# Kernel tuning notes

Hardware: AMD Instinct MI355X
Metric: run time of the kernel (lower is better)

## Reference

```python
import jax, jax.numpy as jnp
import numpy as np
from jax.scipy.linalg import solve_triangular

REG = 1e-6  # reg_covar added to covariance diagonal
LOG2PI = float(np.log(2.0 * np.pi))
RESP_EPS = 10.0 * float(np.finfo(np.float32).eps)


def _log_gauss(X, means, covs):
    # X: [N,D], means: [K,D], covs: [K,D,D] -> per-sample per-component log N(x|mu_k, Sigma_k): [N,K]
    K, D = means.shape
    eye = jnp.eye(D, dtype=X.dtype)
    chol = jnp.linalg.cholesky(covs + REG * eye)                      # [K,D,D]
    diff = X[None, :, :] - means[:, None, :]                          # [K,N,D]
    sol = jax.vmap(lambda L, d: solve_triangular(L, d.T, lower=True))(chol, diff)  # [K,D,N]
    maha = jnp.sum(sol * sol, axis=1)                                 # [K,N]
    logdet = jnp.sum(jnp.log(jnp.diagonal(chol, axis1=1, axis2=2)), axis=1)  # [K] = 0.5*log|Sigma|
    return (-0.5 * (D * LOG2PI + maha) - logdet[:, None]).T           # [N,K]


def _em_step(X, weights, means, covs):
    N, D = X.shape
    # E-step: responsibilities via stable logsumexp
    lp = _log_gauss(X, means, covs) + jnp.log(weights)[None, :]       # [N,K]
    log_norm = jax.scipy.special.logsumexp(lp, axis=1)                # [N]
    resp = jnp.exp(lp - log_norm[:, None])                            # [N,K]
    # M-step (MLE)
    nk = resp.sum(axis=0) + RESP_EPS                                  # [K]
    new_w = nk / N
    new_means = (resp.T @ X) / nk[:, None]                            # [K,D]
    diff = X[None, :, :] - new_means[:, None, :]                      # [K,N,D]
    new_covs = jnp.einsum('kn,knd,kne->kde', resp.T, diff, diff) / nk[:, None, None]
    new_covs = new_covs + REG * jnp.eye(D, dtype=X.dtype)
    return new_w, new_means, new_covs


def reference(X, weights, means, covariances, n_iter):
    # Normalize provided weights (uniform init in the torch module)
    w0 = weights / jnp.sum(weights)

    def step(carry, _):
        w, m, c = carry
        return _em_step(X, w, m, c), None

    (w, m, c), _ = jax.lax.scan(step, (w0, means, covariances), xs=None, length=n_iter)
    # Final per-sample log-likelihood under the fitted mixture (lower bound)
    lp = _log_gauss(X, m, c) + jnp.log(w)[None, :]
    return jax.scipy.special.logsumexp(lp, axis=1)                    # [N]


def setup_inputs() -> dict:
    key = jax.random.key(0)
    kx, km = jax.random.split(key)
    N, D, K = 100000, 32, 16
    X = jax.random.normal(kx, (N, D), dtype=jnp.float32)
    weights = jnp.ones((K,), dtype=jnp.float32) / K
    means = jax.random.normal(km, (K, D), dtype=jnp.float32)
    covariances = jnp.tile(jnp.eye(D, dtype=jnp.float32)[None], (K, 1, 1))
    return {"X": X, "weights": weights, "means": means, "covariances": covariances, "n_iter": 5}
```

## Files before the change

### kernel.cpp

```cpp
#include <hip/hip_runtime.h>
#include <math.h>

#define REGC 1e-6f
#define LOG2PI 1.83787706640934534f
#define RESP_EPS 1.1920929e-6f

#define PART_K 1156
#define RS 16

typedef __attribute__((ext_vector_type(8))) short short8;
typedef __attribute__((ext_vector_type(4))) float f32x4;
typedef unsigned short ushort_t;
typedef unsigned int uint_t;

__device__ __forceinline__ ushort_t f2bf(float x) {
    uint_t u = __float_as_uint(x);
    uint_t r = (u + 0x7fffu + ((u >> 16) & 1u)) >> 16;
    return (ushort_t)r;
}
__device__ __forceinline__ float bf2f(ushort_t h) {
    return __uint_as_float(((uint_t)h) << 16);
}
__device__ __forceinline__ f32x4 shx4(f32x4 v, int m) {
    f32x4 r;
#pragma unroll
    for (int i = 0; i < 4; ++i) r[i] = __shfl_xor(v[i], m);
    return r;
}
__device__ __forceinline__ f32x4 sel4(bool s, f32x4 b, f32x4 a) {
    f32x4 r;
#pragma unroll
    for (int i = 0; i < 4; ++i) r[i] = s ? b[i] : a[i];
    return r;
}
__device__ __forceinline__ short8 pack_rx(const float* r8, const short8 bh, float& row) {
    uint_t u[8];
#pragma unroll
    for (int jj = 0; jj < 8; ++jj) {
        float av = r8[jj] * bf2f((ushort_t)bh[jj]);
        row += av;
        u[jj] = __float_as_uint(av) + 0x8000u;
    }
    short8 out;
    uint_t* o = (uint_t*)&out;
    o[0] = __builtin_amdgcn_perm(u[1], u[0], 0x07060302);
    o[1] = __builtin_amdgcn_perm(u[3], u[2], 0x07060302);
    o[2] = __builtin_amdgcn_perm(u[5], u[4], 0x07060302);
    o[3] = __builtin_amdgcn_perm(u[7], u[6], 0x07060302);
    return out;
}

__global__ __launch_bounds__(256) void gmm_xsplit(const float* __restrict__ X,
                                                  ushort_t* __restrict__ Xh,
                                                  ushort_t* __restrict__ Xl,
                                                  ushort_t* __restrict__ XTH,
                                                  int N) {
    int chunk = blockIdx.x;
    int t = threadIdx.x;
    __shared__ float xsh[32][33];
    int s = t >> 3, q = t & 7;
    int n = chunk * 32 + s;
    float4 v = make_float4(0.f, 0.f, 0.f, 0.f);
    if (n < N) v = ((const float4*)(X + (size_t)n * 32))[q];
    float vv[4] = { v.x, v.y, v.z, v.w };
    xsh[s][q * 4 + 0] = v.x; xsh[s][q * 4 + 1] = v.y;
    xsh[s][q * 4 + 2] = v.z; xsh[s][q * 4 + 3] = v.w;
    if (n < N) {
        ushort_t h[4], l[4];
#pragma unroll
        for (int i = 0; i < 4; ++i) {
            h[i] = f2bf(vv[i]);
            l[i] = f2bf(vv[i] - bf2f(h[i]));
        }
        size_t o = (size_t)n * 32 + q * 4;
        *(uint2*)(Xh + o) = make_uint2((uint_t)h[0] | ((uint_t)h[1] << 16),
                                       (uint_t)h[2] | ((uint_t)h[3] << 16));
        *(uint2*)(Xl + o) = make_uint2((uint_t)l[0] | ((uint_t)l[1] << 16),
                                       (uint_t)l[2] | ((uint_t)l[3] << 16));
    }
    __syncthreads();
    int di = t >> 7;
    int lane = (t >> 1) & 63;
    int jj0 = (t & 1) * 4;
    int c = lane & 15, quad = lane >> 4;
    int d = di * 16 + c;
    ushort_t fh[4];
#pragma unroll
    for (int i = 0; i < 4; ++i) fh[i] = f2bf(xsh[quad * 8 + jj0 + i][d]);
    size_t fo = ((size_t)(chunk * 2 + di) * 64 + lane) * 8 + jj0;
    *(uint2*)(XTH + fo) = make_uint2((uint_t)fh[0] | ((uint_t)fh[1] << 16),
                                     (uint_t)fh[2] | ((uint_t)fh[3] << 16));
}

__global__ __launch_bounds__(64) void gmm_prep0(const float* __restrict__ w,
                                                const float* __restrict__ mu,
                                                const float* __restrict__ cov,
                                                ushort_t* __restrict__ Wh,
                                                ushort_t* __restrict__ Wl,
                                                float* __restrict__ Bv,
                                                float* __restrict__ Cc) {
    int k = blockIdx.x;
    int t = threadIdx.x;
    __shared__ float L[32][33];
    __shared__ float Ai[32][33];
    const float* cv = cov + (size_t)k * 1024;
    const float* muk = mu + (size_t)k * 32;
#pragma unroll
    for (int rep = 0; rep < 16; ++rep) {
        int idx = rep * 64 + t;
        int i = idx >> 5, j = idx & 31;
        L[i][j] = cv[idx] + (i == j ? REGC : 0.f);
    }
    __syncthreads();
#pragma unroll
    for (int j = 0; j < 32; ++j) {
        float s = L[j][j];
#pragma unroll
        for (int p = 0; p < j; ++p) { float v = L[j][p]; s -= v * v; }
        float dj = sqrtf(s);
        if (t > j && t < 32) {
            float s2 = L[t][j];
#pragma unroll
            for (int p = 0; p < j; ++p) s2 -= L[t][p] * L[j][p];
            L[t][j] = s2 / dj;
        }
        if (t == j) L[j][j] = dj;
        __syncthreads();
    }
    if (t < 32) {
        float ai[32];
#pragma unroll
        for (int r = 0; r < 32; ++r) {
            float s = (r == t) ? 1.f : 0.f;
#pragma unroll
            for (int p = 0; p < r; ++p) s -= L[r][p] * ai[p];
            ai[r] = s / L[r][r];
        }
#pragma unroll
        for (int r = 0; r < 32; ++r) Ai[r][t] = ai[r];
    }
    __syncthreads();
#pragma unroll
    for (int rep = 0; rep < 16; ++rep) {
        int idx = rep * 64 + t;
        int i = idx >> 5, j = idx & 31;
        float v = Ai[i][j];
        ushort_t h = f2bf(v);
        Wh[(size_t)(k * 32 + i) * 32 + j] = h;
        Wl[(size_t)(k * 32 + i) * 32 + j] = f2bf(v - bf2f(h));
    }
    if (t < 32) {
        float s = 0.f;
#pragma unroll
        for (int j = 0; j < 32; ++j) s += Ai[t][j] * muk[j];
        Bv[k * 32 + t] = s;
    }
    float wsum = 0.f;
#pragma unroll
    for (int i = 0; i < 16; ++i) wsum += w[i];
    float lv = (t < 32) ? logf(L[t & 31][t & 31]) : 0.f;
#pragma unroll
    for (int off = 1; off < 32; off <<= 1) lv += __shfl_xor(lv, off);
    if (t == 0) Cc[k] = logf(w[k] / wsum) - 0.5f * 32.0f * LOG2PI - lv;
}

__global__ __launch_bounds__(1024) __attribute__((amdgpu_waves_per_eu(4, 4)))
void gmm_emstep(const ushort_t* __restrict__ Xh, const ushort_t* __restrict__ Xl,
                const ushort_t* __restrict__ XTH,
                const ushort_t* __restrict__ Wh, const ushort_t* __restrict__ Wl,
                const float* __restrict__ Bv, const float* __restrict__ Cc,
                float* __restrict__ part, int N) {
    __shared__ float rsh[16][516];
    int t = threadIdx.x;
    int wave = t >> 6, lane = t & 63;
    int quad = lane >> 4, c = lane & 15;

    int wstart0 = (int)blockIdx.x * 512 + wave * 32;
    bool dup = (wstart0 + 32 > N);
    int wst = dup ? ((N >= 32) ? N - 32 : 0) : wstart0;

    size_t xo0 = (size_t)(wst + c) * 32 + quad * 8;
    size_t xo1 = (size_t)(wst + 16 + c) * 32 + quad * 8;
    short8 ah0 = *(const short8*)(Xh + xo0);
    short8 al0 = *(const short8*)(Xl + xo0);
    short8 ah1 = *(const short8*)(Xh + xo1);
    short8 al1 = *(const short8*)(Xl + xo1);

    {
        f32x4 p0[2], p1[2], p2[2], p3[2], fin[2];
#pragma unroll
        for (int k = 0; k < 16; ++k) {
            size_t w0 = (size_t)(k * 32 + c) * 32 + quad * 8;
            size_t w1 = w0 + 512;
            short8 bh0 = *(const short8*)(Wh + w0);
            short8 bl0 = *(const short8*)(Wl + w0);
            short8 bh1 = *(const short8*)(Wh + w1);
            short8 bl1 = *(const short8*)(Wl + w1);
            float bv0 = Bv[k * 32 + c];
            float bv1 = Bv[k * 32 + 16 + c];
#pragma unroll
            for (int tt = 0; tt < 2; ++tt) {
                short8 ah = tt ? ah1 : ah0;
                short8 al = tt ? al1 : al0;
                f32x4 a0 = {0.f, 0.f, 0.f, 0.f};
                f32x4 a1 = {0.f, 0.f, 0.f, 0.f};
                a0 = __builtin_amdgcn_mfma_f32_16x16x32_bf16(ah, bh0, a0, 0, 0, 0);
                a0 = __builtin_amdgcn_mfma_f32_16x16x32_bf16(ah, bl0, a0, 0, 0, 0);
                a0 = __builtin_amdgcn_mfma_f32_16x16x32_bf16(al, bh0, a0, 0, 0, 0);
                a1 = __builtin_amdgcn_mfma_f32_16x16x32_bf16(ah, bh1, a1, 0, 0, 0);
                a1 = __builtin_amdgcn_mfma_f32_16x16x32_bf16(ah, bl1, a1, 0, 0, 0);
                a1 = __builtin_amdgcn_mfma_f32_16x16x32_bf16(al, bh1, a1, 0, 0, 0);
                f32x4 ms;
#pragma unroll
                for (int r = 0; r < 4; ++r) {
                    float d0 = a0[r] - bv0;
                    float d1 = a1[r] - bv1;
                    ms[r] = fmaf(d0, d0, d1 * d1);
                }
                if ((k & 1) == 0) { p0[tt] = ms; }
                else {
                    f32x4 a = p0[tt] + shx4(p0[tt], 1);
                    f32x4 b = ms + shx4(ms, 1);
                    f32x4 v = sel4((c & 1) != 0, b, a);
                    if ((k & 2) == 0) { p1[tt] = v; }
                    else {
                        a = p1[tt] + shx4(p1[tt], 2); b = v + shx4(v, 2); v = sel4((c & 2) != 0, b, a);
                        if ((k & 4) == 0) { p2[tt] = v; }
                        else {
                            a = p2[tt] + shx4(p2[tt], 4); b = v + shx4(v, 4); v = sel4((c & 4) != 0, b, a);
                            if ((k & 8) == 0) { p3[tt] = v; }
                            else {
                                a = p3[tt] + shx4(p3[tt], 8); b = v + shx4(v, 8);
                                fin[tt] = sel4((c & 8) != 0, b, a);
                            }
                        }
                    }
                }
            }
        }
        float ccv = Cc[c];
#pragma unroll
        for (int tt = 0; tt < 2; ++tt) {
            f32x4 lp;
#pragma unroll
            for (int r = 0; r < 4; ++r) lp[r] = ccv - 0.5f * fin[tt][r];
            f32x4 mx = lp;
#pragma unroll
            for (int off = 1; off < 16; off <<= 1) {
                f32x4 s = shx4(mx, off);
#pragma unroll
                for (int r = 0; r < 4; ++r) mx[r] = fmaxf(mx[r], s[r]);
            }
            f32x4 e;
#pragma unroll
            for (int r = 0; r < 4; ++r) e[r] = __expf(lp[r] - mx[r]);
            f32x4 sm = e;
#pragma unroll
            for (int off = 1; off < 16; off <<= 1) sm = sm + shx4(sm, off);
            f32x4 sv;
#pragma unroll
            for (int r = 0; r < 4; ++r) sv[r] = dup ? 0.f : e[r] / sm[r];
            *(f32x4*)&rsh[c][wave * 32 + tt * 16 + quad * 4] = sv;
        }
    }
    __syncthreads();

    {
        int k = wave;
        f32x4 m00 = {0.f,0.f,0.f,0.f}, m01 = {0.f,0.f,0.f,0.f};
        f32x4 m10 = {0.f,0.f,0.f,0.f}, m11 = {0.f,0.f,0.f,0.f};
        float row0 = 0.f, row1 = 0.f, corner = 0.f;
#pragma unroll 4
        for (int ch = 0; ch < 16; ++ch) {
            size_t fb = (((size_t)((int)blockIdx.x * 16 + ch)) * 128 + lane) * 8;
            short8 bh0 = *(const short8*)(XTH + fb);
            short8 bh1 = *(const short8*)(XTH + fb + 512);
            float r8[8];
#pragma unroll
            for (int jj = 0; jj < 8; ++jj) r8[jj] = rsh[k][ch * 32 + quad * 8 + jj];
            corner += ((r8[0]+r8[1])+(r8[2]+r8[3])) + ((r8[4]+r8[5])+(r8[6]+r8[7]));
            short8 a0 = pack_rx(r8, bh0, row0);
            short8 a1 = pack_rx(r8, bh1, row1);
            m00 = __builtin_amdgcn_mfma_f32_16x16x32_bf16(a0, bh0, m00, 0, 0, 0);
            m01 = __builtin_amdgcn_mfma_f32_16x16x32_bf16(a0, bh1, m01, 0, 0, 0);
            m10 = __builtin_amdgcn_mfma_f32_16x16x32_bf16(a1, bh0, m10, 0, 0, 0);
            m11 = __builtin_amdgcn_mfma_f32_16x16x32_bf16(a1, bh1, m11, 0, 0, 0);
        }
        row0 += __shfl_xor(row0, 16);  row0 += __shfl_xor(row0, 32);
        row1 += __shfl_xor(row1, 16);  row1 += __shfl_xor(row1, 32);
        corner += __shfl_xor(corner, 16);  corner += __shfl_xor(corner, 32);

        float* pb = part + ((size_t)blockIdx.x * 16 + k) * PART_K;
#pragma unroll
        for (int r = 0; r < 4; ++r) {
            pb[(quad * 4 + r) * 34 + c]           = m00[r];
            pb[(quad * 4 + r) * 34 + 16 + c]      = m01[r];
            pb[(16 + quad * 4 + r) * 34 + c]      = m10[r];
            pb[(16 + quad * 4 + r) * 34 + 16 + c] = m11[r];
        }
        if (quad == 0) {
            pb[32 * 34 + c]      = row0;
            pb[32 * 34 + 16 + c] = row1;
        }
        if (lane == 0) pb[32 * 34 + 32] = corner;
    }
}

__global__ __launch_bounds__(256) void gmm_reduce1(const float* __restrict__ part,
                                                   float* __restrict__ part2,
                                                   int npart) {
    int k = blockIdx.x, g = blockIdx.y;
    int nb = (npart + RS - 1) / RS;
    int b0 = g * nb;
    int b1 = b0 + nb; if (b1 > npart) b1 = npart;
    for (int idx = threadIdx.x; idx < PART_K; idx += 256) {
        float s = 0.f;
#pragma unroll 4
        for (int b = b0; b < b1; ++b)
            s += part[((size_t)b * 16 + k) * PART_K + idx];
        part2[((size_t)g * 16 + k) * PART_K + idx] = s;
    }
}

__global__ __launch_bounds__(1024) void gmm_redfin_prep(const float* __restrict__ part2,
                                                        ushort_t* __restrict__ Wh,
                                                        ushort_t* __restrict__ Wl,
                                                        float* __restrict__ Bv,
                                                        float* __restrict__ Cc,
                                                        int N) {
    int k = blockIdx.x;
    int t = threadIdx.x;
    __shared__ float S[1156];
    __shared__ float L[1056];
    __shared__ float Ai[1056];
    __shared__ float mean[32];

    for (int idx = t; idx < 1121; idx += 1024) {
        float s = 0.f;
#pragma unroll
        for (int b = 0; b < RS; ++b)
            s += part2[((size_t)b * 16 + k) * PART_K + idx];
        S[idx] = s;
    }
    __syncthreads();
    float nk = S[32 * 34 + 32] + RESP_EPS;
    float inv = 1.f / nk;
    {
        int i = t >> 5, j = t & 31;
        float mi = S[32 * 34 + i] * inv;
        float mj = S[32 * 34 + j] * inv;
        L[i * 33 + j] = S[i * 34 + j] * inv - mi * mj + ((i == j) ? 2.f * REGC : 0.f);
    }
    if (t < 32) mean[t] = S[32 * 34 + t] * inv;
    __syncthreads();

#pragma unroll
    for (int j = 0; j < 32; ++j) {
        if (t < 32) {
            float s = L[j * 33 + j];
#pragma unroll
            for (int p = 0; p < j; ++p) { float v = L[j * 33 + p]; s -= v * v; }
            float dj = sqrtf(s);
            if (t > j) {
                float s2 = L[t * 33 + j];
#pragma unroll
                for (int p = 0; p < j; ++p) s2 -= L[t * 33 + p] * L[j * 33 + p];
                L[t * 33 + j] = s2 / dj;
            }
            if (t == j) L[j * 33 + j] = dj;
        }
        __syncthreads();
    }
    if (t < 32) {
        float ai[32];
#pragma unroll
        for (int r = 0; r < 32; ++r) {
            float s = (r == t) ? 1.f : 0.f;
#pragma unroll
            for (int p = 0; p < r; ++p) s -= L[r * 33 + p] * ai[p];
            ai[r] = s / L[r * 33 + r];
        }
#pragma unroll
        for (int r = 0; r < 32; ++r) Ai[r * 33 + t] = ai[r];
    }
    __syncthreads();
    {
        int i = t >> 5, j = t & 31;
        float v = Ai[i * 33 + j];
        ushort_t h = f2bf(v);
        Wh[(size_t)(k * 32 + i) * 32 + j] = h;
        Wl[(size_t)(k * 32 + i) * 32 + j] = f2bf(v - bf2f(h));
    }
    if (t < 32) {
        float s = 0.f;
#pragma unroll
        for (int j = 0; j < 32; ++j) s += Ai[t * 33 + j] * mean[j];
        Bv[k * 32 + t] = s;
    }
    float lv = (t < 32) ? logf(L[(t & 31) * 33 + (t & 31)]) : 0.f;
#pragma unroll
    for (int off = 1; off < 32; off <<= 1) lv += __shfl_xor(lv, off);
    if (t == 0) Cc[k] = logf(nk / (float)N) - 0.5f * 32.0f * LOG2PI - lv;
}

__global__ __launch_bounds__(256, 2) void gmm_estep_fin(const ushort_t* __restrict__ Xh,
                                                        const ushort_t* __restrict__ Xl,
                                                        const ushort_t* __restrict__ Wh,
                                                        const ushort_t* __restrict__ Wl,
                                                        const float* __restrict__ Bv,
                                                        const float* __restrict__ Cc,
                                                        float* __restrict__ out,
                                                        int N) {
    int t = threadIdx.x;
    int wave = t >> 6, lane = t & 63;
    int quad = lane >> 4, c = lane & 15;
    int wstart = (blockIdx.x * 4 + wave) * 32;
    if (wstart + 32 > N) wstart = (N >= 32) ? (N - 32) : 0;
    bool al4 = ((N & 3) == 0);

    size_t xo0 = (size_t)(wstart + c) * 32 + quad * 8;
    size_t xo1 = (size_t)(wstart + 16 + c) * 32 + quad * 8;
    short8 ah0 = *(const short8*)(Xh + xo0);
    short8 al0 = *(const short8*)(Xl + xo0);
    short8 ah1 = *(const short8*)(Xh + xo1);
    short8 al1 = *(const short8*)(Xl + xo1);

    f32x4 p0[2], p1[2], p2[2], p3[2], fin[2];
#pragma unroll
    for (int k = 0; k < 16; ++k) {
        size_t w0 = (size_t)(k * 32 + c) * 32 + quad * 8;
        size_t w1 = w0 + 512;
        short8 bh0 = *(const short8*)(Wh + w0);
        short8 bl0 = *(const short8*)(Wl + w0);
        short8 bh1 = *(const short8*)(Wh + w1);
        short8 bl1 = *(const short8*)(Wl + w1);
        float bv0 = Bv[k * 32 + c];
        float bv1 = Bv[k * 32 + 16 + c];
#pragma unroll
        for (int tt = 0; tt < 2; ++tt) {
            short8 ah = tt ? ah1 : ah0;
            short8 al = tt ? al1 : al0;
            f32x4 a0 = {0.f, 0.f, 0.f, 0.f};
            f32x4 a1 = {0.f, 0.f, 0.f, 0.f};
            a0 = __builtin_amdgcn_mfma_f32_16x16x32_bf16(ah, bh0, a0, 0, 0, 0);
            a0 = __builtin_amdgcn_mfma_f32_16x16x32_bf16(ah, bl0, a0, 0, 0, 0);
            a0 = __builtin_amdgcn_mfma_f32_16x16x32_bf16(al, bh0, a0, 0, 0, 0);
            a1 = __builtin_amdgcn_mfma_f32_16x16x32_bf16(ah, bh1, a1, 0, 0, 0);
            a1 = __builtin_amdgcn_mfma_f32_16x16x32_bf16(ah, bl1, a1, 0, 0, 0);
            a1 = __builtin_amdgcn_mfma_f32_16x16x32_bf16(al, bh1, a1, 0, 0, 0);
            f32x4 ms;
#pragma unroll
            for (int r = 0; r < 4; ++r) {
                float d0 = a0[r] - bv0;
                float d1 = a1[r] - bv1;
                ms[r] = fmaf(d0, d0, d1 * d1);
            }
            if ((k & 1) == 0) { p0[tt] = ms; }
            else {
                f32x4 a = p0[tt] + shx4(p0[tt], 1);
                f32x4 b = ms + shx4(ms, 1);
                f32x4 v = sel4((c & 1) != 0, b, a);
                if ((k & 2) == 0) { p1[tt] = v; }
                else {
                    a = p1[tt] + shx4(p1[tt], 2); b = v + shx4(v, 2); v = sel4((c & 2) != 0, b, a);
                    if ((k & 4) == 0) { p2[tt] = v; }
                    else {
                        a = p2[tt] + shx4(p2[tt], 4); b = v + shx4(v, 4); v = sel4((c & 4) != 0, b, a);
                        if ((k & 8) == 0) { p3[tt] = v; }
                        else {
                            a = p3[tt] + shx4(p3[tt], 8); b = v + shx4(v, 8);
                            fin[tt] = sel4((c & 8) != 0, b, a);
                        }
                    }
                }
            }
        }
    }
    float ccv = Cc[c];
#pragma unroll
    for (int tt = 0; tt < 2; ++tt) {
        f32x4 lp;
#pragma unroll
        for (int r = 0; r < 4; ++r) lp[r] = ccv - 0.5f * fin[tt][r];
        f32x4 mx = lp;
#pragma unroll
        for (int off = 1; off < 16; off <<= 1) {
            f32x4 s = shx4(mx, off);
#pragma unroll
            for (int r = 0; r < 4; ++r) mx[r] = fmaxf(mx[r], s[r]);
        }
        f32x4 e;
#pragma unroll
        for (int r = 0; r < 4; ++r) e[r] = __expf(lp[r] - mx[r]);
        f32x4 sm = e;
#pragma unroll
        for (int off = 1; off < 16; off <<= 1) sm = sm + shx4(sm, off);
        if (c == 0) {
            int nb = wstart + tt * 16 + quad * 4;
            f32x4 o;
#pragma unroll
            for (int r = 0; r < 4; ++r) o[r] = mx[r] + __logf(sm[r]);
            if (al4) *(f32x4*)(out + nb) = o;
            else { for (int r = 0; r < 4; ++r) out[nb + r] = o[r]; }
        }
    }
}

extern "C" void kernel_launch(void* const* d_in, const int* in_sizes, int n_in,
                              void* d_out, int out_size, void* d_ws, size_t ws_size,
                              hipStream_t stream) {
    const float* X   = (const float*)d_in[0];
    const float* w   = (const float*)d_in[1];
    const float* mu  = (const float*)d_in[2];
    const float* cov = (const float*)d_in[3];
    const int NITER = 5;
    int N = in_sizes[0] / 32;
    int NB = (N + 511) / 512;
    int NCB = NB * 16;

    float* ws = (float*)d_ws;
    float*    Bv = ws;
    float*    Cc = ws + 512;
    ushort_t* Wh = (ushort_t*)(ws + 528);
    ushort_t* Wl = (ushort_t*)(ws + 8720);
    ushort_t* Xh = (ushort_t*)(ws + 16912);
    ushort_t* Xl = (ushort_t*)(ws + 16912 + (size_t)16 * N);
    size_t xt0 = 16912 + (size_t)32 * N;
    size_t SZ  = (size_t)NCB * 512;
    ushort_t* XTH = (ushort_t*)(ws + xt0);
    float*  part2 = ws + xt0 + SZ;
    float*  part  = part2 + (size_t)RS * 16 * PART_K;

    float* out = (float*)d_out;

    int eblocks = ((N + 31) / 32 + 3) / 4;

    gmm_xsplit<<<NCB, 256, 0, stream>>>(X, Xh, Xl, XTH, N);
    gmm_prep0<<<16, 64, 0, stream>>>(w, mu, cov, Wh, Wl, Bv, Cc);

    for (int it = 0; it < NITER; ++it) {
        gmm_emstep<<<NB, 1024, 0, stream>>>(Xh, Xl, XTH, Wh, Wl, Bv, Cc, part, N);
        dim3 r1(16, RS);
        gmm_reduce1<<<r1, 256, 0, stream>>>(part, part2, NB);
        gmm_redfin_prep<<<16, 1024, 0, stream>>>(part2, Wh, Wl, Bv, Cc, N);
    }
    gmm_estep_fin<<<eblocks, 256, 0, stream>>>(Xh, Xl, Wh, Wl, Bv, Cc, out, N);
}
```

Measured before the change: 455.0 us.

## Halve per-block sample tile and fuse partial reduction with covariance finalize

The EM-step kernel now processes 256 samples per block (16 per wave) instead of 512, which doubles the grid size and halves per-wave register state and shared scratch. The two post-reduction kernels are merged into one, where the last-arriving block per component (tracked via an atomic counter) does the final sum, Cholesky and inverse. This removes a kernel launch per iteration and aims to fill more compute units. In exchange the number of partial sums to reduce doubles, and the counter must be reset correctly between launches.

```diff
diff --git a/kernel.cpp b/kernel.cpp
--- a/kernel.cpp
+++ b/kernel.cpp
@@ -98,13 +98,15 @@
                                                 ushort_t* __restrict__ Wh,
                                                 ushort_t* __restrict__ Wl,
                                                 float* __restrict__ Bv,
-                                                float* __restrict__ Cc) {
+                                                float* __restrict__ Cc,
+                                                uint_t* __restrict__ cnt) {
     int k = blockIdx.x;
     int t = threadIdx.x;
     __shared__ float L[32][33];
     __shared__ float Ai[32][33];
     const float* cv = cov + (size_t)k * 1024;
     const float* muk = mu + (size_t)k * 32;
+    if (t == 0) cnt[k] = 0u;
 #pragma unroll
     for (int rep = 0; rep < 16; ++rep) {
         int idx = rep * 64 + t;
@@ -164,30 +166,27 @@
     if (t == 0) Cc[k] = logf(w[k] / wsum) - 0.5f * 32.0f * LOG2PI - lv;
 }
 
-__global__ __launch_bounds__(1024) __attribute__((amdgpu_waves_per_eu(4, 4)))
+__global__ __launch_bounds__(1024) __attribute__((amdgpu_waves_per_eu(8)))
 void gmm_emstep(const ushort_t* __restrict__ Xh, const ushort_t* __restrict__ Xl,
                 const ushort_t* __restrict__ XTH,
                 const ushort_t* __restrict__ Wh, const ushort_t* __restrict__ Wl,
                 const float* __restrict__ Bv, const float* __restrict__ Cc,
                 float* __restrict__ part, int N) {
-    __shared__ float rsh[16][516];
+    __shared__ float rsh[16][264];
     int t = threadIdx.x;
     int wave = t >> 6, lane = t & 63;
     int quad = lane >> 4, c = lane & 15;
 
-    int wstart0 = (int)blockIdx.x * 512 + wave * 32;
-    bool dup = (wstart0 + 32 > N);
-    int wst = dup ? ((N >= 32) ? N - 32 : 0) : wstart0;
-
-    size_t xo0 = (size_t)(wst + c) * 32 + quad * 8;
-    size_t xo1 = (size_t)(wst + 16 + c) * 32 + quad * 8;
-    short8 ah0 = *(const short8*)(Xh + xo0);
-    short8 al0 = *(const short8*)(Xl + xo0);
-    short8 ah1 = *(const short8*)(Xh + xo1);
-    short8 al1 = *(const short8*)(Xl + xo1);
-
     {
-        f32x4 p0[2], p1[2], p2[2], p3[2], fin[2];
+        int wstart0 = (int)blockIdx.x * 256 + wave * 16;
+        bool dup = (wstart0 + 16 > N);
+        int wst = dup ? ((N >= 16) ? N - 16 : 0) : wstart0;
+
+        size_t xo = (size_t)(wst + c) * 32 + quad * 8;
+        short8 ah = *(const short8*)(Xh + xo);
+        short8 al = *(const short8*)(Xl + xo);
+
+        f32x4 p0, p1, p2, p3, fin;
 #pragma unroll
         for (int k = 0; k < 16; ++k) {
             size_t w0 = (size_t)(k * 32 + c) * 32 + quad * 8;
@@ -198,70 +197,62 @@
             short8 bl1 = *(const short8*)(Wl + w1);
             float bv0 = Bv[k * 32 + c];
             float bv1 = Bv[k * 32 + 16 + c];
-#pragma unroll
-            for (int tt = 0; tt < 2; ++tt) {
-                short8 ah = tt ? ah1 : ah0;
-                short8 al = tt ? al1 : al0;
-                f32x4 a0 = {0.f, 0.f, 0.f, 0.f};
-                f32x4 a1 = {0.f, 0.f, 0.f, 0.f};
-                a0 = __builtin_amdgcn_mfma_f32_16x16x32_bf16(ah, bh0, a0, 0, 0, 0);
-                a0 = __builtin_amdgcn_mfma_f32_16x16x32_bf16(ah, bl0, a0, 0, 0, 0);
-                a0 = __builtin_amdgcn_mfma_f32_16x16x32_bf16(al, bh0, a0, 0, 0, 0);
-                a1 = __builtin_amdgcn_mfma_f32_16x16x32_bf16(ah, bh1, a1, 0, 0, 0);
-                a1 = __builtin_amdgcn_mfma_f32_16x16x32_bf16(ah, bl1, a1, 0, 0, 0);
-                a1 = __builtin_amdgcn_mfma_f32_16x16x32_bf16(al, bh1, a1, 0, 0, 0);
-                f32x4 ms;
-#pragma unroll
-                for (int r = 0; r < 4; ++r) {
-                    float d0 = a0[r] - bv0;
-                    float d1 = a1[r] - bv1;
-                    ms[r] = fmaf(d0, d0, d1 * d1);
-                }
-                if ((k & 1) == 0) { p0[tt] = ms; }
+            f32x4 a0 = {0.f, 0.f, 0.f, 0.f};
+            f32x4 a1 = {0.f, 0.f, 0.f, 0.f};
+            a0 = __builtin_amdgcn_mfma_f32_16x16x32_bf16(ah, bh0, a0, 0, 0, 0);
+            a0 = __builtin_amdgcn_mfma_f32_16x16x32_bf16(ah, bl0, a0, 0, 0, 0);
+            a0 = __builtin_amdgcn_mfma_f32_16x16x32_bf16(al, bh0, a0, 0, 0, 0);
+            a1 = __builtin_amdgcn_mfma_f32_16x16x32_bf16(ah, bh1, a1, 0, 0, 0);
+            a1 = __builtin_amdgcn_mfma_f32_16x16x32_bf16(ah, bl1, a1, 0, 0, 0);
+            a1 = __builtin_amdgcn_mfma_f32_16x16x32_bf16(al, bh1, a1, 0, 0, 0);
+            f32x4 ms;
+#pragma unroll
+            for (int r = 0; r < 4; ++r) {
+                float d0 = a0[r] - bv0;
+                float d1 = a1[r] - bv1;
+                ms[r] = fmaf(d0, d0, d1 * d1);
+            }
+            if ((k & 1) == 0) { p0 = ms; }
+            else {
+                f32x4 a = p0 + shx4(p0, 1);
+                f32x4 b = ms + shx4(ms, 1);
+                f32x4 v = sel4((c & 1) != 0, b, a);
+                if ((k & 2) == 0) { p1 = v; }
                 else {
-                    f32x4 a = p0[tt] + shx4(p0[tt], 1);
-                    f32x4 b = ms + shx4(ms, 1);
-                    f32x4 v = sel4((c & 1) != 0, b, a);
-                    if ((k & 2) == 0) { p1[tt] = v; }
+                    a = p1 + shx4(p1, 2); b = v + shx4(v, 2); v = sel4((c & 2) != 0, b, a);
+                    if ((k & 4) == 0) { p2 = v; }
                     else {
-                        a = p1[tt] + shx4(p1[tt], 2); b = v + shx4(v, 2); v = sel4((c & 2) != 0, b, a);
-                        if ((k & 4) == 0) { p2[tt] = v; }
+                        a = p2 + shx4(p2, 4); b = v + shx4(v, 4); v = sel4((c & 4) != 0, b, a);
+                        if ((k & 8) == 0) { p3 = v; }
                         else {
-                            a = p2[tt] + shx4(p2[tt], 4); b = v + shx4(v, 4); v = sel4((c & 4) != 0, b, a);
-                            if ((k & 8) == 0) { p3[tt] = v; }
-                            else {
-                                a = p3[tt] + shx4(p3[tt], 8); b = v + shx4(v, 8);
-                                fin[tt] = sel4((c & 8) != 0, b, a);
-                            }
+                            a = p3 + shx4(p3, 8); b = v + shx4(v, 8);
+                            fin = sel4((c & 8) != 0, b, a);
                         }
                     }
                 }
             }
         }
         float ccv = Cc[c];
-#pragma unroll
-        for (int tt = 0; tt < 2; ++tt) {
-            f32x4 lp;
-#pragma unroll
-            for (int r = 0; r < 4; ++r) lp[r] = ccv - 0.5f * fin[tt][r];
-            f32x4 mx = lp;
-#pragma unroll
-            for (int off = 1; off < 16; off <<= 1) {
-                f32x4 s = shx4(mx, off);
-#pragma unroll
-                for (int r = 0; r < 4; ++r) mx[r] = fmaxf(mx[r], s[r]);
-            }
-            f32x4 e;
-#pragma unroll
-            for (int r = 0; r < 4; ++r) e[r] = __expf(lp[r] - mx[r]);
-            f32x4 sm = e;
-#pragma unroll
-            for (int off = 1; off < 16; off <<= 1) sm = sm + shx4(sm, off);
-            f32x4 sv;
-#pragma unroll
-            for (int r = 0; r < 4; ++r) sv[r] = dup ? 0.f : e[r] / sm[r];
-            *(f32x4*)&rsh[c][wave * 32 + tt * 16 + quad * 4] = sv;
-        }
+        f32x4 lp;
+#pragma unroll
+        for (int r = 0; r < 4; ++r) lp[r] = ccv - 0.5f * fin[r];
+        f32x4 mx = lp;
+#pragma unroll
+        for (int off = 1; off < 16; off <<= 1) {
+            f32x4 s = shx4(mx, off);
+#pragma unroll
+            for (int r = 0; r < 4; ++r) mx[r] = fmaxf(mx[r], s[r]);
+        }
+        f32x4 e;
+#pragma unroll
+        for (int r = 0; r < 4; ++r) e[r] = __expf(lp[r] - mx[r]);
+        f32x4 sm = e;
+#pragma unroll
+        for (int off = 1; off < 16; off <<= 1) sm = sm + shx4(sm, off);
+        f32x4 sv;
+#pragma unroll
+        for (int r = 0; r < 4; ++r) sv[r] = dup ? 0.f : e[r] / sm[r];
+        *(f32x4*)&rsh[c][wave * 16 + quad * 4] = sv;
     }
     __syncthreads();
 
@@ -270,9 +261,9 @@
         f32x4 m00 = {0.f,0.f,0.f,0.f}, m01 = {0.f,0.f,0.f,0.f};
         f32x4 m10 = {0.f,0.f,0.f,0.f}, m11 = {0.f,0.f,0.f,0.f};
         float row0 = 0.f, row1 = 0.f, corner = 0.f;
-#pragma unroll 4
-        for (int ch = 0; ch < 16; ++ch) {
-            size_t fb = (((size_t)((int)blockIdx.x * 16 + ch)) * 128 + lane) * 8;
+#pragma unroll 2
+        for (int ch = 0; ch < 8; ++ch) {
+            size_t fb = (((size_t)((int)blockIdx.x * 8 + ch)) * 128 + lane) * 8;
             short8 bh0 = *(const short8*)(XTH + fb);
             short8 bh1 = *(const short8*)(XTH + fb + 512);
             float r8[8];
@@ -306,36 +297,40 @@
     }
 }
 
-__global__ __launch_bounds__(256) void gmm_reduce1(const float* __restrict__ part,
-                                                   float* __restrict__ part2,
-                                                   int npart) {
+__global__ __launch_bounds__(256) void gmm_reduce_fin(const float* __restrict__ part,
+                                                      float* __restrict__ part2,
+                                                      ushort_t* __restrict__ Wh,
+                                                      ushort_t* __restrict__ Wl,
+                                                      float* __restrict__ Bv,
+                                                      float* __restrict__ Cc,
+                                                      uint_t* __restrict__ cnt,
+                                                      int N, int npart) {
     int k = blockIdx.x, g = blockIdx.y;
+    int t = threadIdx.x;
+    __shared__ float S[1156];
+    __shared__ float L[32][33];
+    __shared__ float Ai[32][33];
+    __shared__ int lastf;
+
     int nb = (npart + RS - 1) / RS;
     int b0 = g * nb;
     int b1 = b0 + nb; if (b1 > npart) b1 = npart;
-    for (int idx = threadIdx.x; idx < PART_K; idx += 256) {
+    for (int idx = t; idx < PART_K; idx += 256) {
         float s = 0.f;
 #pragma unroll 4
         for (int b = b0; b < b1; ++b)
             s += part[((size_t)b * 16 + k) * PART_K + idx];
         part2[((size_t)g * 16 + k) * PART_K + idx] = s;
     }
-}
-
-__global__ __launch_bounds__(1024) void gmm_redfin_prep(const float* __restrict__ part2,
-                                                        ushort_t* __restrict__ Wh,
-                                                        ushort_t* __restrict__ Wl,
-                                                        float* __restrict__ Bv,
-                                                        float* __restrict__ Cc,
-                                                        int N) {
-    int k = blockIdx.x;
-    int t = threadIdx.x;
-    __shared__ float S[1156];
-    __shared__ float L[1056];
-    __shared__ float Ai[1056];
-    __shared__ float mean[32];
-
-    for (int idx = t; idx < 1121; idx += 1024) {
+    __threadfence();
+    __syncthreads();
+    if (t == 0) lastf = (atomicAdd(&cnt[k], 1u) == (uint_t)(RS - 1));
+    __syncthreads();
+    if (!lastf) return;
+    if (t == 0) cnt[k] = 0u;
+    __threadfence();
+
+    for (int idx = t; idx < 1121; idx += 256) {
         float s = 0.f;
 #pragma unroll
         for (int b = 0; b < RS; ++b)
@@ -345,29 +340,27 @@
     __syncthreads();
     float nk = S[32 * 34 + 32] + RESP_EPS;
     float inv = 1.f / nk;
-    {
-        int i = t >> 5, j = t & 31;
+    for (int idx = t; idx < 1024; idx += 256) {
+        int i = idx >> 5, j = idx & 31;
         float mi = S[32 * 34 + i] * inv;
         float mj = S[32 * 34 + j] * inv;
-        L[i * 33 + j] = S[i * 34 + j] * inv - mi * mj + ((i == j) ? 2.f * REGC : 0.f);
-    }
-    if (t < 32) mean[t] = S[32 * 34 + t] * inv;
-    __syncthreads();
-
+        L[i][j] = S[i * 34 + j] * inv - mi * mj + ((i == j) ? 2.f * REGC : 0.f);
+    }
+    __syncthreads();
 #pragma unroll
     for (int j = 0; j < 32; ++j) {
         if (t < 32) {
-            float s = L[j * 33 + j];
-#pragma unroll
-            for (int p = 0; p < j; ++p) { float v = L[j * 33 + p]; s -= v * v; }
+            float s = L[j][j];
+#pragma unroll
+            for (int p = 0; p < j; ++p) { float v = L[j][p]; s -= v * v; }
             float dj = sqrtf(s);
             if (t > j) {
-                float s2 = L[t * 33 + j];
-#pragma unroll
-                for (int p = 0; p < j; ++p) s2 -= L[t * 33 + p] * L[j * 33 + p];
-                L[t * 33 + j] = s2 / dj;
+                float s2 = L[t][j];
+#pragma unroll
+                for (int p = 0; p < j; ++p) s2 -= L[t][p] * L[j][p];
+                L[t][j] = s2 / dj;
             }
-            if (t == j) L[j * 33 + j] = dj;
+            if (t == j) L[j][j] = dj;
         }
         __syncthreads();
     }
@@ -377,16 +370,18 @@
         for (int r = 0; r < 32; ++r) {
             float s = (r == t) ? 1.f : 0.f;
 #pragma unroll
-            for (int p = 0; p < r; ++p) s -= L[r * 33 + p] * ai[p];
-            ai[r] = s / L[r * 33 + r];
-        }
-#pragma unroll
-        for (int r = 0; r < 32; ++r) Ai[r * 33 + t] = ai[r];
-    }
-    __syncthreads();
-    {
-        int i = t >> 5, j = t & 31;
-        float v = Ai[i * 33 + j];
+            for (int p = 0; p < r; ++p) s -= L[r][p] * ai[p];
+            ai[r] = s / L[r][r];
+        }
+#pragma unroll
+        for (int r = 0; r < 32; ++r) Ai[r][t] = ai[r];
+    }
+    __syncthreads();
+#pragma unroll
+    for (int rep = 0; rep < 4; ++rep) {
+        int idx = rep * 256 + t;
+        int i = idx >> 5, j = idx & 31;
+        float v = Ai[i][j];
         ushort_t h = f2bf(v);
         Wh[(size_t)(k * 32 + i) * 32 + j] = h;
         Wl[(size_t)(k * 32 + i) * 32 + j] = f2bf(v - bf2f(h));
@@ -394,10 +389,10 @@
     if (t < 32) {
         float s = 0.f;
 #pragma unroll
-        for (int j = 0; j < 32; ++j) s += Ai[t * 33 + j] * mean[j];
+        for (int j = 0; j < 32; ++j) s += Ai[t][j] * (S[32 * 34 + j] * inv);
         Bv[k * 32 + t] = s;
     }
-    float lv = (t < 32) ? logf(L[(t & 31) * 33 + (t & 31)]) : 0.f;
+    float lv = (t < 32) ? logf(L[t & 31][t & 31]) : 0.f;
 #pragma unroll
     for (int off = 1; off < 32; off <<= 1) lv += __shfl_xor(lv, off);
     if (t == 0) Cc[k] = logf(nk / (float)N) - 0.5f * 32.0f * LOG2PI - lv;
@@ -515,34 +510,33 @@
     const float* cov = (const float*)d_in[3];
     const int NITER = 5;
     int N = in_sizes[0] / 32;
-    int NB = (N + 511) / 512;
-    int NCB = NB * 16;
+    int NB = (N + 255) / 256;
+    int NCB = NB * 8;
 
     float* ws = (float*)d_ws;
-    float*    Bv = ws;
-    float*    Cc = ws + 512;
-    ushort_t* Wh = (ushort_t*)(ws + 528);
-    ushort_t* Wl = (ushort_t*)(ws + 8720);
-    ushort_t* Xh = (ushort_t*)(ws + 16912);
-    ushort_t* Xl = (ushort_t*)(ws + 16912 + (size_t)16 * N);
-    size_t xt0 = 16912 + (size_t)32 * N;
+    float*    Bv  = ws;
+    float*    Cc  = ws + 512;
+    uint_t*   cnt = (uint_t*)(ws + 528);
+    ushort_t* Wh  = (ushort_t*)(ws + 544);
+    ushort_t* Wl  = (ushort_t*)(ws + 8736);
+    ushort_t* Xh  = (ushort_t*)(ws + 16928);
+    ushort_t* Xl  = (ushort_t*)(ws + 16928 + (size_t)16 * N);
+    size_t xt0 = 16928 + (size_t)32 * N;
     size_t SZ  = (size_t)NCB * 512;
     ushort_t* XTH = (ushort_t*)(ws + xt0);
     float*  part2 = ws + xt0 + SZ;
     float*  part  = part2 + (size_t)RS * 16 * PART_K;
 
     float* out = (float*)d_out;
-
     int eblocks = ((N + 31) / 32 + 3) / 4;
 
     gmm_xsplit<<<NCB, 256, 0, stream>>>(X, Xh, Xl, XTH, N);
-    gmm_prep0<<<16, 64, 0, stream>>>(w, mu, cov, Wh, Wl, Bv, Cc);
+    gmm_prep0<<<16, 64, 0, stream>>>(w, mu, cov, Wh, Wl, Bv, Cc, cnt);
 
     for (int it = 0; it < NITER; ++it) {
         gmm_emstep<<<NB, 1024, 0, stream>>>(Xh, Xl, XTH, Wh, Wl, Bv, Cc, part, N);
-        dim3 r1(16, RS);
-        gmm_reduce1<<<r1, 256, 0, stream>>>(part, part2, NB);
-        gmm_redfin_prep<<<16, 1024, 0, stream>>>(part2, Wh, Wl, Bv, Cc, N);
+        dim3 rf(16, RS);
+        gmm_reduce_fin<<<rf, 256, 0, stream>>>(part, part2, Wh, Wl, Bv, Cc, cnt, N, NB);
     }
     gmm_estep_fin<<<eblocks, 256, 0, stream>>>(Xh, Xl, Wh, Wl, Bv, Cc, out, N);
 }
```

Measured after the change: 644.6 us. 41.7% more time.
